# Kernel tuning notes

Hardware: AMD Instinct MI355X
Metric: run time of the kernel (lower is better)

The kernel has to match this reference:

```python
import jax, jax.numpy as jnp
import numpy as np

USER = 100000
ITEM = 100000
LATDIM = 64
ETYPE = 8
GNN_LAYERS = 2
HYPER_NUM = 128
N_EDGES = 100000


def setup_inputs() -> dict:
    key = jax.random.key(0)
    ks = jax.random.split(key, 7)
    # xavier-ish scaled params
    uEmbeds = jax.random.normal(ks[0], (USER, LATDIM), dtype=jnp.float32) * 0.05
    iEmbeds = jax.random.normal(ks[1], (ITEM, LATDIM), dtype=jnp.float32) * 0.05
    edgeTrans = jax.random.normal(ks[2], (ETYPE, LATDIM, LATDIM), dtype=jnp.float32) * 0.1
    src = jax.random.randint(ks[3], (N_EDGES,), 0, USER, dtype=jnp.int64 if jax.config.jax_enable_x64 else jnp.int32)
    tgt = jax.random.randint(ks[4], (N_EDGES,), 0, ITEM, dtype=src.dtype)
    val = jax.random.randint(ks[5], (N_EDGES,), 0, ETYPE, dtype=src.dtype)
    hyper = jax.random.normal(ks[6], (N_EDGES, HYPER_NUM), dtype=jnp.float32)
    return {"uEmbeds": uEmbeds, "iEmbeds": iEmbeds, "edgeTrans": edgeTrans,
            "hyper": hyper, "src": src, "tgt": tgt, "val": val}


def _hgnn_layer(edgeEmbeds, hyper):
    act = lambda x: jax.nn.leaky_relu(x, 0.5)
    # [d, H] = embeds^T @ hyper
    hyperEmbeds = act(jnp.einsum('ed,eh->dh', edgeEmbeds, hyper))
    # [E, d] = (hyperEmbeds @ hyper^T)^T
    nodeEmbeds = act(jnp.einsum('eh,dh->ed', hyper, hyperEmbeds))
    return nodeEmbeds


def reference(uEmbeds, iEmbeds, edgeTrans, hyper, src, tgt, val):
    srcE = uEmbeds[src]                       # [E, d] gather
    trans = edgeTrans[val]                    # [E, d, d] gather (large)
    # per-edge row-vector x matrix, then elementwise mult with tgt embeds
    edgeEmbeds = jnp.einsum('ed,edk->ek', srcE, trans) * iEmbeds[tgt]  # [E, d]
    for _ in range(GNN_LAYERS):
        edgeEmbeds = _hgnn_layer(edgeEmbeds, hyper) + edgeEmbeds
    srcOut = jax.ops.segment_sum(edgeEmbeds, src, num_segments=USER)  # sparse.sum over dim 1
    tgtOut = jax.ops.segment_sum(edgeEmbeds, tgt, num_segments=ITEM)  # sparse.sum over dim 0
    return (srcOut, tgtOut)
```

## Files before the change

kernel.cpp:

```cpp
#include <hip/hip_runtime.h>

#define E_N     100000
#define USER_N  100000
#define NROW    200000
#define NB_ACC  256
#define BIN_CAP 16384
#define E_PAD   114688
#define ACC_NCH 7
#define ACC_CHUNK 64
#define BUCKET_CAP 16
#define NB_INIT 782

typedef __bf16 bf16x8 __attribute__((ext_vector_type(8)));
typedef __bf16 bf16x4 __attribute__((ext_vector_type(4)));
typedef float  f32x4  __attribute__((ext_vector_type(4)));

__device__ __forceinline__ float leaky(float x) { return x > 0.f ? x : 0.5f * x; }

__global__ void initKernel(int* __restrict__ cnt, int* __restrict__ cnt8,
                           const float* __restrict__ T, __bf16* __restrict__ Tt) {
  const int b = blockIdx.x;
  const int i = b * 256 + threadIdx.x;
  if (i < NROW + 2) cnt[i] = 0;
  if (i < 8) cnt8[i] = 0;
  if (b < 8) {
    const float* Tv = T + (size_t)b * 4096;
    __bf16* Tb = Tt + (size_t)b * 4096;
    for (int idx = threadIdx.x; idx < 4096; idx += 256) {
      const int d = idx >> 6, k = idx & 63;
      Tb[k * 64 + d] = (__bf16)Tv[idx];
    }
  }
}

__global__ void binKernel(const int* __restrict__ val, const int* __restrict__ src,
                          const int* __restrict__ tgt,
                          int* __restrict__ perm, int* __restrict__ permSrc,
                          int* __restrict__ permTgt,
                          int* __restrict__ cnt8, int* __restrict__ cnt,
                          int* __restrict__ list) {
  __shared__ int lh[8], lbase[8];
  const int tid = threadIdx.x;
  if (tid < 8) lh[tid] = 0;
  __syncthreads();
  const int e = blockIdx.x * 256 + tid;
  int v = -1, slot = 0, s = 0, t = 0;
  if (e < E_N) {
    v = val[e]; s = src[e]; t = tgt[e];
    slot = atomicAdd(&lh[v], 1);
    const int ps = atomicAdd(&cnt[s], 1);
    if (ps < BUCKET_CAP) list[(size_t)s * BUCKET_CAP + ps] = e;
    const int pt = atomicAdd(&cnt[USER_N + t], 1);
    if (pt < BUCKET_CAP) list[(size_t)(USER_N + t) * BUCKET_CAP + pt] = e;
  }
  __syncthreads();
  if (tid < 8) lbase[tid] = atomicAdd(&cnt8[tid], lh[tid]);
  __syncthreads();
  if (v >= 0) {
    const int p = v * BIN_CAP + lbase[v] + slot;
    perm[p] = e; permSrc[p] = s; permTgt[p] = t;
  }
}

__global__ void __launch_bounds__(256) convertHyperTKernel(const float* __restrict__ hyper,
                                                           __bf16* __restrict__ hyperT,
                                                           __bf16* __restrict__ hyperB) {
  __shared__ __bf16 sT[128][72];
  const int tid = threadIdx.x;
  const int e0 = blockIdx.x * 64;
  const int h = tid >> 1, eoff = (tid & 1) * 32;
  if (e0 >= E_N) {
    const float4 z = make_float4(0.f, 0.f, 0.f, 0.f);
    #pragma unroll
    for (int q = 0; q < 4; ++q)
      *(float4*)((char*)(hyperT + (size_t)h * E_PAD + e0 + eoff) + q * 16) = z;
    return;
  }
  #pragma unroll
  for (int r = 0; r < 8; ++r) {
    const int idx = r * 256 + tid;
    const int e = idx >> 5, h4 = (idx & 31) * 4;
    float4 v = make_float4(0.f, 0.f, 0.f, 0.f);
    if (e0 + e < E_N) {
      v = *(const float4*)(hyper + (size_t)(e0 + e) * 128 + h4);
      bf16x4 pk;
      pk[0] = (__bf16)v.x; pk[1] = (__bf16)v.y; pk[2] = (__bf16)v.z; pk[3] = (__bf16)v.w;
      *(bf16x4*)(hyperB + (size_t)(e0 + e) * 128 + h4) = pk;
    }
    sT[h4 + 0][e] = (__bf16)v.x; sT[h4 + 1][e] = (__bf16)v.y;
    sT[h4 + 2][e] = (__bf16)v.z; sT[h4 + 3][e] = (__bf16)v.w;
  }
  __syncthreads();
  #pragma unroll
  for (int q = 0; q < 8; ++q) {
    const bf16x4 v = *(const bf16x4*)&sT[h][eoff + q * 4];
    *(bf16x4*)(hyperT + (size_t)h * E_PAD + e0 + eoff + q * 4) = v;
  }
}

__global__ void __launch_bounds__(256) stageAMfmaKernel(
    const float* __restrict__ uE, const float* __restrict__ iE, const __bf16* __restrict__ Tt,
    const int* __restrict__ permSrc, const int* __restrict__ permTgt,
    const int* __restrict__ perm, const int* __restrict__ cnt8,
    float* __restrict__ edge) {
  const int v  = blockIdx.y;
  const int nE = min(cnt8[v], BIN_CAP);
  if (blockIdx.x * 64 >= nE) return;
  const int tid  = threadIdx.x;
  const int lane = tid & 63;
  const int wave = tid >> 6;
  const int l16 = lane & 15, quad = lane >> 4;
  const int t0 = blockIdx.x * 64 + wave * 16;
  if (t0 >= nE) return;

  bf16x8 Bf[2][4];
  #pragma unroll
  for (int kc = 0; kc < 2; ++kc)
    #pragma unroll
    for (int nt = 0; nt < 4; ++nt)
      Bf[kc][nt] = *(const bf16x8*)(Tt + (size_t)v * 4096 + (nt * 16 + l16) * 64 + kc * 32 + quad * 8);

  const int pbase = v * BIN_CAP + t0;
  const bool liveRow = (t0 + l16 < nE);
  const int sIdx = liveRow ? permSrc[pbase + l16] : 0;
  const int tIdx = liveRow ? permTgt[pbase + l16] : 0;
  const int eIdx = liveRow ? perm[pbase + l16]    : 0;

  bf16x8 A[2];
  #pragma unroll
  for (int kc = 0; kc < 2; ++kc) {
    const float* ap = uE + (size_t)sIdx * 64 + kc * 32 + quad * 8;
    const float4 f0 = *(const float4*)ap;
    const float4 f1 = *(const float4*)(ap + 4);
    bf16x8 a;
    a[0] = (__bf16)f0.x; a[1] = (__bf16)f0.y; a[2] = (__bf16)f0.z; a[3] = (__bf16)f0.w;
    a[4] = (__bf16)f1.x; a[5] = (__bf16)f1.y; a[6] = (__bf16)f1.z; a[7] = (__bf16)f1.w;
    A[kc] = a;
  }

  f32x4 acc[4];
  #pragma unroll
  for (int nt = 0; nt < 4; ++nt) acc[nt] = (f32x4){0.f, 0.f, 0.f, 0.f};
  #pragma unroll
  for (int kc = 0; kc < 2; ++kc)
    #pragma unroll
    for (int nt = 0; nt < 4; ++nt)
      acc[nt] = __builtin_amdgcn_mfma_f32_16x16x32_bf16(A[kc], Bf[kc][nt], acc[nt], 0, 0, 0);

  const int qb = lane & 48;
  #pragma unroll
  for (int reg = 0; reg < 4; ++reg) {
    const int j  = quad * 4 + reg;
    const int tj = __shfl(tIdx, qb | j, 64);
    const int gj = __shfl(eIdx, qb | j, 64);
    if (t0 + j < nE) {
      #pragma unroll
      for (int nt = 0; nt < 4; ++nt) {
        const int k = nt * 16 + l16;
        edge[(size_t)gj * 64 + k] = acc[nt][reg] * iE[(size_t)tj * 64 + k];
      }
    }
  }
}

__global__ void __launch_bounds__(512) hyperAccumMfmaKernel(
    const float* __restrict__ edge, const __bf16* __restrict__ hyperT,
    float* __restrict__ partials) {
  __shared__ __bf16 sE[2][64][72];
  const int tid  = threadIdx.x;
  const int lane = tid & 63;
  const int wave = tid >> 6;
  const int l16 = lane & 15, quad = lane >> 4;
  const int e0base = blockIdx.x * (ACC_NCH * ACC_CHUNK);
  const int d  = tid & 63;
  const int eg = tid >> 6;

  float rv[8];
  auto gload = [&](int c) {
    const int ebase = e0base + c * ACC_CHUNK + eg * 8;
    const float* p = edge + (size_t)ebase * 64 + d;
    if (ebase + 8 <= E_N) {
      #pragma unroll
      for (int i = 0; i < 8; ++i) rv[i] = p[i * 64];
    } else {
      #pragma unroll
      for (int i = 0; i < 8; ++i) rv[i] = (ebase + i < E_N) ? p[i * 64] : 0.f;
    }
  };
  auto swrite = [&](int b) {
    bf16x8 pk;
    #pragma unroll
    for (int i = 0; i < 8; ++i) pk[i] = (__bf16)rv[i];
    *(bf16x8*)&sE[b][d][eg * 8] = pk;
  };

  f32x4 acc[4];
  #pragma unroll
  for (int dt = 0; dt < 4; ++dt) acc[dt] = (f32x4){0.f, 0.f, 0.f, 0.f};

  gload(0); swrite(0);
  __syncthreads();
  for (int c = 0; c < ACC_NCH; ++c) {
    const int nb = c & 1;
    if (c + 1 < ACC_NCH) gload(c + 1);
    #pragma unroll
    for (int ks = 0; ks < 2; ++ks) {
      const int eoff = c * ACC_CHUNK + ks * 32 + quad * 8;
      const bf16x8 B = *(const bf16x8*)(hyperT + (size_t)(wave * 16 + l16) * E_PAD + e0base + eoff);
      bf16x8 A[4];
      #pragma unroll
      for (int dt = 0; dt < 4; ++dt)
        A[dt] = *(const bf16x8*)&sE[nb][dt * 16 + l16][ks * 32 + quad * 8];
      #pragma unroll
      for (int dt = 0; dt < 4; ++dt)
        acc[dt] = __builtin_amdgcn_mfma_f32_16x16x32_bf16(A[dt], B, acc[dt], 0, 0, 0);
    }
    if (c + 1 < ACC_NCH) {
      __syncthreads();
      swrite(nb ^ 1);
      __syncthreads();
    }
  }
  float* pp = partials + (size_t)blockIdx.x * 8192;
  const int h = wave * 16 + l16;
  #pragma unroll
  for (int dt = 0; dt < 4; ++dt)
    #pragma unroll
    for (int reg = 0; reg < 4; ++reg) {
      const int dd = dt * 16 + quad * 4 + reg;
      pp[dd * 128 + h] = acc[dt][reg];
    }
}

__global__ void __launch_bounds__(256) reduceKernel(const float* __restrict__ partials,
                                                    __bf16* __restrict__ HEtT) {
  __shared__ float sd[8][33];
  const int tid = threadIdx.x;
  const int o = blockIdx.x * 32 + (tid & 31);
  const int g = tid >> 5;
  float s = 0.f;
  #pragma unroll 4
  for (int b = g * 32; b < (g + 1) * 32; ++b) s += partials[(size_t)b * 8192 + o];
  sd[g][tid & 31] = s;
  __syncthreads();
  if (tid < 32) {
    float t = 0.f;
    #pragma unroll
    for (int k = 0; k < 8; ++k) t += sd[k][tid];
    HEtT[blockIdx.x * 32 + tid] = (__bf16)leaky(t);
  }
}

__global__ void __launch_bounds__(256) nodeUpdateMfmaKernel(
    const __bf16* __restrict__ HEtT, const __bf16* __restrict__ hyperB,
    float* __restrict__ edge) {
  const int tid  = threadIdx.x;
  const int lane = tid & 63;
  const int wave = tid >> 6;
  const int l16 = lane & 15, quad = lane >> 4;
  bf16x8 Bf[4][4];
  #pragma unroll
  for (int kc = 0; kc < 4; ++kc)
    #pragma unroll
    for (int dt = 0; dt < 4; ++dt)
      Bf[kc][dt] = *(const bf16x8*)(HEtT + (dt * 16 + l16) * 128 + kc * 32 + quad * 8);
  const int wv = blockIdx.x * 4 + wave;
  for (int t = wv; t < E_N / 16; t += 2048) {
    const int e0 = t * 16;
    bf16x8 A[4];
    #pragma unroll
    for (int kc = 0; kc < 4; ++kc)
      A[kc] = *(const bf16x8*)(hyperB + (size_t)(e0 + l16) * 128 + kc * 32 + quad * 8);
    f32x4 acc[4];
    #pragma unroll
    for (int dt = 0; dt < 4; ++dt) acc[dt] = (f32x4){0.f, 0.f, 0.f, 0.f};
    #pragma unroll
    for (int kc = 0; kc < 4; ++kc)
      #pragma unroll
      for (int dt = 0; dt < 4; ++dt)
        acc[dt] = __builtin_amdgcn_mfma_f32_16x16x32_bf16(A[kc], Bf[kc][dt], acc[dt], 0, 0, 0);
    #pragma unroll
    for (int dt = 0; dt < 4; ++dt) {
      const int d = dt * 16 + l16;
      #pragma unroll
      for (int reg = 0; reg < 4; ++reg) {
        const int e = e0 + quad * 4 + reg;
        float* ep = edge + (size_t)e * 64 + d;
        *ep = *ep + leaky(acc[dt][reg]);
      }
    }
  }
}

__global__ void gatherSumKernel(const float* __restrict__ edge,
                                const int* __restrict__ cnt,
                                const int* __restrict__ list,
                                float* __restrict__ out) {
  const int tid = threadIdx.x;
  const int sub = tid & 15;
  const int grpInWave = (tid >> 4) & 3;
  const int gid = blockIdx.x * 16 + (tid >> 4);
  const int nG = gridDim.x * 16;
  for (int r = gid; r < NROW; r += nG) {
    const int n = min(cnt[r], BUCKET_CAP);
    int eL = (sub < n) ? list[(size_t)r * BUCKET_CAP + sub] : 0;
    float4 acc = make_float4(0.f, 0.f, 0.f, 0.f);
    for (int i = 0; i < n; ++i) {
      const int e = __shfl(eL, grpInWave * 16 + i, 64);
      const float4 v = *(const float4*)(edge + (size_t)e * 64 + sub * 4);
      acc.x += v.x; acc.y += v.y; acc.z += v.z; acc.w += v.w;
    }
    *(float4*)(out + (size_t)r * 64 + sub * 4) = acc;
  }
}

extern "C" void kernel_launch(void* const* d_in, const int* in_sizes, int n_in,
                              void* d_out, int out_size, void* d_ws, size_t ws_size,
                              hipStream_t stream) {
  const float* uE    = (const float*)d_in[0];
  const float* iE    = (const float*)d_in[1];
  const float* T     = (const float*)d_in[2];
  const float* hyper = (const float*)d_in[3];
  const int*   src   = (const int*)d_in[4];
  const int*   tgt   = (const int*)d_in[5];
  const int*   val   = (const int*)d_in[6];
  float* out = (float*)d_out;
  float* ws  = (float*)d_ws;

  float*  edge     = ws;
  float*  partials = ws + 6400000;
  __bf16* HEtT     = (__bf16*)(ws + 6400000 + 4194304 + 65536);
  int* perm    = (int*)partials;
  int* permSrc = perm + 8 * BIN_CAP;
  int* permTgt = permSrc + 8 * BIN_CAP;
  int* cnt8    = permTgt + 8 * BIN_CAP;
  int* cnt  = (int*)(ws + 6400000 + 4194304 + 65536 + 4096);
  int* list = cnt + (NROW + 4);
  __bf16* hyperT = (__bf16*)(ws + 15136256);
  __bf16* hyperB = (__bf16*)(ws + 22476288);
  __bf16* Tt     = (__bf16*)(ws + 28876288);

  initKernel<<<NB_INIT, 256, 0, stream>>>(cnt, cnt8, T, Tt);
  binKernel<<<(E_N + 255) / 256, 256, 0, stream>>>(val, src, tgt, perm, permSrc, permTgt, cnt8, cnt, list);
  convertHyperTKernel<<<E_PAD / 64, 256, 0, stream>>>(hyper, hyperT, hyperB);
  stageAMfmaKernel<<<dim3(BIN_CAP / 64, 8), 256, 0, stream>>>(uE, iE, Tt, permSrc, permTgt, perm, cnt8, edge);

  for (int layer = 0; layer < 2; ++layer) {
    hyperAccumMfmaKernel<<<NB_ACC, 512, 0, stream>>>(edge, hyperT, partials);
    reduceKernel<<<256, 256, 0, stream>>>(partials, HEtT);
    nodeUpdateMfmaKernel<<<512, 256, 0, stream>>>(HEtT, hyperB, edge);
  }

  gatherSumKernel<<<6250, 256, 0, stream>>>(edge, cnt, list, out);
}
```

Before: 285.1 us.

## Process four edge tiles per wave in stage A with LDS-staged vectorized stores

The stage A kernel now has each wave handle 64 edges (four 16-row MFMA tiles) instead of 16, so the transform fragments loaded per wave are reused across four tiles. The MFMA outputs are staged through shared memory so that each lane writes float4 rows and reads the target embeddings as float4, replacing scattered scalar stores. The gather-sum launch count is also doubled. This costs more registers and LDS and gives fewer blocks, which may reduce occupancy.

```diff
diff --git a/kernel.cpp b/kernel.cpp
--- a/kernel.cpp
+++ b/kernel.cpp
@@ -103,15 +103,15 @@
     const int* __restrict__ permSrc, const int* __restrict__ permTgt,
     const int* __restrict__ perm, const int* __restrict__ cnt8,
     float* __restrict__ edge) {
+  __shared__ float sC[4][16][68];
   const int v  = blockIdx.y;
   const int nE = min(cnt8[v], BIN_CAP);
-  if (blockIdx.x * 64 >= nE) return;
   const int tid  = threadIdx.x;
   const int lane = tid & 63;
   const int wave = tid >> 6;
   const int l16 = lane & 15, quad = lane >> 4;
-  const int t0 = blockIdx.x * 64 + wave * 16;
-  if (t0 >= nE) return;
+  const int wbase = blockIdx.x * 256 + wave * 64;
+  if (wbase >= nE) return;
 
   bf16x8 Bf[2][4];
   #pragma unroll
@@ -120,44 +120,71 @@
     for (int nt = 0; nt < 4; ++nt)
       Bf[kc][nt] = *(const bf16x8*)(Tt + (size_t)v * 4096 + (nt * 16 + l16) * 64 + kc * 32 + quad * 8);
 
-  const int pbase = v * BIN_CAP + t0;
-  const bool liveRow = (t0 + l16 < nE);
-  const int sIdx = liveRow ? permSrc[pbase + l16] : 0;
-  const int tIdx = liveRow ? permTgt[pbase + l16] : 0;
-  const int eIdx = liveRow ? perm[pbase + l16]    : 0;
-
-  bf16x8 A[2];
-  #pragma unroll
-  for (int kc = 0; kc < 2; ++kc) {
-    const float* ap = uE + (size_t)sIdx * 64 + kc * 32 + quad * 8;
-    const float4 f0 = *(const float4*)ap;
-    const float4 f1 = *(const float4*)(ap + 4);
-    bf16x8 a;
-    a[0] = (__bf16)f0.x; a[1] = (__bf16)f0.y; a[2] = (__bf16)f0.z; a[3] = (__bf16)f0.w;
-    a[4] = (__bf16)f1.x; a[5] = (__bf16)f1.y; a[6] = (__bf16)f1.z; a[7] = (__bf16)f1.w;
-    A[kc] = a;
-  }
-
-  f32x4 acc[4];
-  #pragma unroll
-  for (int nt = 0; nt < 4; ++nt) acc[nt] = (f32x4){0.f, 0.f, 0.f, 0.f};
-  #pragma unroll
-  for (int kc = 0; kc < 2; ++kc)
-    #pragma unroll
-    for (int nt = 0; nt < 4; ++nt)
-      acc[nt] = __builtin_amdgcn_mfma_f32_16x16x32_bf16(A[kc], Bf[kc][nt], acc[nt], 0, 0, 0);
-
-  const int qb = lane & 48;
-  #pragma unroll
-  for (int reg = 0; reg < 4; ++reg) {
-    const int j  = quad * 4 + reg;
-    const int tj = __shfl(tIdx, qb | j, 64);
-    const int gj = __shfl(eIdx, qb | j, 64);
-    if (t0 + j < nE) {
-      #pragma unroll
-      for (int nt = 0; nt < 4; ++nt) {
-        const int k = nt * 16 + l16;
-        edge[(size_t)gj * 64 + k] = acc[nt][reg] * iE[(size_t)tj * 64 + k];
+  int sI[4], tI[4], eI[4];
+  #pragma unroll
+  for (int s = 0; s < 4; ++s) {
+    const int eoffS = wbase + s * 16;
+    const bool lv = (eoffS + l16 < nE);
+    const int p = v * BIN_CAP + (lv ? eoffS + l16 : 0);
+    sI[s] = permSrc[p]; tI[s] = permTgt[p]; eI[s] = perm[p];
+  }
+
+  float4 f0[4][2], f1[4][2];
+  #pragma unroll
+  for (int s = 0; s < 4; ++s)
+    #pragma unroll
+    for (int kc = 0; kc < 2; ++kc) {
+      const float* ap = uE + (size_t)sI[s] * 64 + kc * 32 + quad * 8;
+      f0[s][kc] = *(const float4*)ap;
+      f1[s][kc] = *(const float4*)(ap + 4);
+    }
+
+  #pragma unroll
+  for (int pr = 0; pr < 2; ++pr) {
+    f32x4 acc[2][4];
+    #pragma unroll
+    for (int sh = 0; sh < 2; ++sh)
+      #pragma unroll
+      for (int nt = 0; nt < 4; ++nt) acc[sh][nt] = (f32x4){0.f, 0.f, 0.f, 0.f};
+    #pragma unroll
+    for (int sh = 0; sh < 2; ++sh) {
+      const int s = pr * 2 + sh;
+      #pragma unroll
+      for (int kc = 0; kc < 2; ++kc) {
+        bf16x8 a;
+        a[0] = (__bf16)f0[s][kc].x; a[1] = (__bf16)f0[s][kc].y;
+        a[2] = (__bf16)f0[s][kc].z; a[3] = (__bf16)f0[s][kc].w;
+        a[4] = (__bf16)f1[s][kc].x; a[5] = (__bf16)f1[s][kc].y;
+        a[6] = (__bf16)f1[s][kc].z; a[7] = (__bf16)f1[s][kc].w;
+        #pragma unroll
+        for (int nt = 0; nt < 4; ++nt)
+          acc[sh][nt] = __builtin_amdgcn_mfma_f32_16x16x32_bf16(a, Bf[kc][nt], acc[sh][nt], 0, 0, 0);
+      }
+    }
+    #pragma unroll
+    for (int sh = 0; sh < 2; ++sh) {
+      const int s = pr * 2 + sh;
+      const int eoffS = wbase + s * 16;
+      #pragma unroll
+      for (int nt = 0; nt < 4; ++nt)
+        #pragma unroll
+        for (int reg = 0; reg < 4; ++reg)
+          sC[wave][quad * 4 + reg][nt * 16 + l16] = acc[sh][nt][reg];
+      const int r  = lane >> 2;
+      const int c0 = (lane & 3) * 4;
+      const int tj = __shfl(tI[s], r, 64);
+      const int gj = __shfl(eI[s], r, 64);
+      if (eoffS + r < nE) {
+        #pragma unroll
+        for (int q = 0; q < 4; ++q) {
+          const int c = c0 + q * 16;
+          const float4 cv = *(const float4*)&sC[wave][r][c];
+          const float4 iv = *(const float4*)(iE + (size_t)tj * 64 + c);
+          float4 rr;
+          rr.x = cv.x * iv.x; rr.y = cv.y * iv.y;
+          rr.z = cv.z * iv.z; rr.w = cv.w * iv.w;
+          *(float4*)(edge + (size_t)gj * 64 + c) = rr;
+        }
       }
     }
   }
@@ -343,7 +370,7 @@
   initKernel<<<NB_INIT, 256, 0, stream>>>(cnt, cnt8, T, Tt);
   binKernel<<<(E_N + 255) / 256, 256, 0, stream>>>(val, src, tgt, perm, permSrc, permTgt, cnt8, cnt, list);
   convertHyperTKernel<<<E_PAD / 64, 256, 0, stream>>>(hyper, hyperT, hyperB);
-  stageAMfmaKernel<<<dim3(BIN_CAP / 64, 8), 256, 0, stream>>>(uE, iE, Tt, permSrc, permTgt, perm, cnt8, edge);
+  stageAMfmaKernel<<<dim3(BIN_CAP / 256, 8), 256, 0, stream>>>(uE, iE, Tt, permSrc, permTgt, perm, cnt8, edge);
 
   for (int layer = 0; layer < 2; ++layer) {
     hyperAccumMfmaKernel<<<NB_ACC, 512, 0, stream>>>(edge, hyperT, partials);
@@ -351,5 +378,5 @@
     nodeUpdateMfmaKernel<<<512, 256, 0, stream>>>(HEtT, hyperB, edge);
   }
 
-  gatherSumKernel<<<6250, 256, 0, stream>>>(edge, cnt, list, out);
-}
+  gatherSumKernel<<<12500, 256, 0, stream>>>(edge, cnt, list, out);
+}
```

After: 283.5 us. Within noise of the previous version (-0.6%).
